# Kernel optimization log

Measured on AMD Instinct MI355X. Metric: run time of the kernel, lower is better.

The kernel has to match this reference:

```python
import jax, jax.numpy as jnp
import numpy as np

N = 50000   # nodes
E = 800000  # edges
D = 256     # in = hidden = out channels
R = 16      # num_relations (last index reserved for self-loops)
B = 8       # num_bases
LN_EPS = 1e-5


def setup_inputs() -> dict:
    key = jax.random.key(0)
    ks = jax.random.split(key, 20)
    s_basis = np.sqrt(2.0 / (D + D)).astype(np.float32)  # glorot-ish scale
    s_att = np.sqrt(2.0 / (R + B)).astype(np.float32)
    inp = {
        "x": jax.random.normal(ks[0], (N, D), dtype=jnp.float32),
        "edge_index": jax.random.randint(ks[1], (2, E), 0, N),
        "edge_type": jax.random.randint(ks[2], (E,), 0, R),
        "edge_attr": jax.random.uniform(ks[3], (E,), dtype=jnp.float32),
        # layer 1 params
        "basis1": jax.random.normal(ks[4], (B, D, D), dtype=jnp.float32) * s_basis,
        "att1": jax.random.normal(ks[5], (R, B), dtype=jnp.float32) * s_att,
        "root1": jax.random.normal(ks[6], (D, D), dtype=jnp.float32) * s_basis,
        "bias1": jnp.zeros((D,), dtype=jnp.float32),
        "ln1_g": jnp.ones((D,), dtype=jnp.float32),
        "ln1_b": jnp.zeros((D,), dtype=jnp.float32),
        # layer 2 params
        "basis2": jax.random.normal(ks[7], (B, D, D), dtype=jnp.float32) * s_basis,
        "att2": jax.random.normal(ks[8], (R, B), dtype=jnp.float32) * s_att,
        "root2": jax.random.normal(ks[9], (D, D), dtype=jnp.float32) * s_basis,
        "bias2": jnp.zeros((D,), dtype=jnp.float32),
        "ln2_g": jnp.ones((D,), dtype=jnp.float32),
        "ln2_b": jnp.zeros((D,), dtype=jnp.float32),
    }
    return inp


def _layer_norm(x, g, b):
    mu = jnp.mean(x, axis=-1, keepdims=True)
    var = jnp.mean(jnp.square(x - mu), axis=-1, keepdims=True)
    return (x - mu) * jax.lax.rsqrt(var + LN_EPS) * g + b


def _rgcn_layer(x, edge_index, edge_type, edge_attr, basis, att, root, bias):
    n = x.shape[0]
    r = att.shape[0]
    # W_r = sum_b a_rb V_b ; then per-relation transform of every node.
    weight = jnp.einsum('rb,bio->rio', att, basis)          # [R, D, D]
    H = jnp.einsum('ni,rio->nro', x, weight)                # [N, R, D]
    # append self-loops with relation index R-1 and confidence 1.0
    loop = jnp.arange(n, dtype=edge_index.dtype)
    src = jnp.concatenate([edge_index[0], loop])
    dst = jnp.concatenate([edge_index[1], loop])
    et = jnp.concatenate([edge_type, jnp.full((n,), r - 1, dtype=edge_type.dtype)])
    ea = jnp.concatenate([edge_attr, jnp.ones((n,), dtype=x.dtype)])
    msg = H[src, et] * ea[:, None]                          # [E+N, D]
    summ = jax.ops.segment_sum(msg, dst, num_segments=n)
    cnt = jax.ops.segment_sum(jnp.ones_like(ea), dst, num_segments=n)
    agg = summ / cnt[:, None]                               # scatter-mean (cnt >= 1 via self-loops)
    return agg + x @ root + bias


def reference(x, edge_index, edge_type, edge_attr,
              basis1, att1, root1, bias1, ln1_g, ln1_b,
              basis2, att2, root2, bias2, ln2_g, ln2_b):
    # input_proj / output_proj are Identity since in == hidden == out.
    h = x
    h_out = _rgcn_layer(h, edge_index, edge_type, edge_attr, basis1, att1, root1, bias1)
    h = jax.nn.relu(_layer_norm(h + h_out, ln1_g, ln1_b))
    h_out = _rgcn_layer(h, edge_index, edge_type, edge_attr, basis2, att2, root2, bias2)
    h = jax.nn.relu(_layer_norm(h + h_out, ln2_g, ln2_b))
    return h
```

## Files before the change

kernel.cpp:

```cpp
#include <hip/hip_runtime.h>
#include <stdint.h>

#define D 256
#define RREL 16
#define BB 8
#define K9 2304
#define KG 2048
#define LN_EPS 1e-5f
#define NT (K9 / 64)
#define BUFB 49152

typedef __attribute__((ext_vector_type(8))) short frag8;
typedef __attribute__((ext_vector_type(4))) float floatx4;
typedef __attribute__((ext_vector_type(2))) float float2v;

__device__ __forceinline__ unsigned short f2bf(float f) {
    union { float f; uint32_t u; } v; v.f = f;
    uint32_t r = (v.u + 0x7FFFu + ((v.u >> 16) & 1u)) >> 16;
    return (unsigned short)r;
}
__device__ __forceinline__ float bf2f(unsigned short u) {
    union { uint32_t u; float f; } v; v.u = (uint32_t)u << 16;
    return v.f;
}
__device__ __forceinline__ float2v bfpair(uint32_t d) {
    union { uint32_t u; float f; } lo, hi;
    lo.u = d << 16; hi.u = d & 0xFFFF0000u;
    return (float2v){lo.f, hi.f};
}

__device__ __forceinline__ float2v pk_mul(float2v a, float2v b) {
    float2v d;
    asm("v_pk_mul_f32 %0, %1, %2" : "=v"(d) : "v"(a), "v"(b));
    return d;
}
__device__ __forceinline__ void pk_fma_lo(float2v& acc, float2v c, float2v x) {
    asm("v_pk_fma_f32 %0, %1, %2, %0 op_sel:[0,0,0] op_sel_hi:[1,0,1]"
        : "+v"(acc) : "v"(c), "v"(x));
}
__device__ __forceinline__ void pk_fma_hi(float2v& acc, float2v c, float2v x) {
    asm("v_pk_fma_f32 %0, %1, %2, %0 op_sel:[0,1,0] op_sel_hi:[1,1,1]"
        : "+v"(acc) : "v"(c), "v"(x));
}

__device__ __forceinline__ void gl2lds16(const unsigned short* g, char* l) {
    __builtin_amdgcn_global_load_lds((const __attribute__((address_space(1))) void*)g,
                                     (__attribute__((address_space(3))) void*)l, 16, 0, 0);
}

__global__ __launch_bounds__(256) void k_cvt(const float* __restrict__ src,
                                             unsigned short* __restrict__ dst, int n4) {
    int i = blockIdx.x * 256 + threadIdx.x;
    if (i >= n4) return;
    float4 v = ((const float4*)src)[i];
    ushort4 o = make_ushort4(f2bf(v.x), f2bf(v.y), f2bf(v.z), f2bf(v.w));
    ((ushort4*)dst)[i] = o;
}

__global__ __launch_bounds__(256) void k_deg(const int* __restrict__ ei,
                                             int* __restrict__ deg, int E) {
    int t = blockIdx.x * 256 + threadIdx.x;
    int stride = gridDim.x * 256;
    int d[8];
#pragma unroll
    for (int j = 0; j < 8; ++j) {
        int e = t + j * stride;
        d[j] = (e < E) ? ei[E + e] : -1;
    }
#pragma unroll
    for (int j = 0; j < 8; ++j)
        if (d[j] >= 0) atomicAdd(&deg[d[j]], 1);
}

__global__ __launch_bounds__(256) void k_scan1(const int* __restrict__ deg,
                                               int* __restrict__ csum, int N) {
    __shared__ int sh[256];
    int n = blockIdx.x * 256 + threadIdx.x;
    sh[threadIdx.x] = (n < N) ? deg[n] : 0;
    __syncthreads();
    for (int off = 128; off > 0; off >>= 1) {
        if (threadIdx.x < off) sh[threadIdx.x] += sh[threadIdx.x + off];
        __syncthreads();
    }
    if (threadIdx.x == 0) csum[blockIdx.x] = sh[0];
}

__global__ __launch_bounds__(256) void k_scan3(const int* __restrict__ deg,
                                               const int* __restrict__ csum, int nch,
                                               int* __restrict__ rowptr,
                                               int* __restrict__ cursor,
                                               float* __restrict__ cnt, int N) {
    __shared__ int sh[256];
    int tid = threadIdx.x;
    int bid = blockIdx.x;
    int base;
    if (nch <= 256) {
        int c = (tid < nch) ? csum[tid] : 0;
        sh[tid] = c;
        __syncthreads();
        for (int off = 1; off < 256; off <<= 1) {
            int t = (tid >= off) ? sh[tid - off] : 0;
            __syncthreads();
            sh[tid] += t;
            __syncthreads();
        }
        base = sh[bid] - csum[bid];
        if (bid == 0 && tid == 255) rowptr[N] = sh[255];
        __syncthreads();
    } else {
        int s = 0;
        for (int i = 0; i < bid; ++i) s += csum[i];
        base = s;
        if (bid == 0 && tid == 0) {
            int tot = 0;
            for (int i = 0; i < nch; ++i) tot += csum[i];
            rowptr[N] = tot;
        }
    }
    int n = bid * 256 + tid;
    int v = (n < N) ? deg[n] : 0;
    sh[tid] = v;
    __syncthreads();
    for (int off = 1; off < 256; off <<= 1) {
        int t = (tid >= off) ? sh[tid - off] : 0;
        __syncthreads();
        sh[tid] += t;
        __syncthreads();
    }
    int excl = sh[tid] - v + base;
    if (n < N) {
        rowptr[n] = excl;
        cursor[n] = excl;
        cnt[n] = (float)(v + 1);
    }
}

__global__ __launch_bounds__(256) void k_scatter(const int* __restrict__ ei,
                                                 const int* __restrict__ et,
                                                 const float* __restrict__ ea,
                                                 int* __restrict__ cursor,
                                                 int2* __restrict__ ep, int E) {
    int t = blockIdx.x * 256 + threadIdx.x;
    int stride = gridDim.x * 256;
    int src[8], dst[8], typ[8]; float w[8]; bool v[8];
#pragma unroll
    for (int j = 0; j < 8; ++j) {
        int e = t + j * stride;
        v[j] = (e < E);
        if (v[j]) { src[j] = ei[e]; dst[j] = ei[E + e]; typ[j] = et[e]; w[j] = ea[e]; }
    }
    int p[8];
#pragma unroll
    for (int j = 0; j < 8; ++j)
        if (v[j]) p[j] = atomicAdd(&cursor[dst[j]], 1);
#pragma unroll
    for (int j = 0; j < 8; ++j)
        if (v[j]) ep[p[j]] = make_int2(src[j] | (typ[j] << 24), __float_as_int(w[j]));
}

__global__ __launch_bounds__(256) void k_prep_w(const float* __restrict__ basis,
                                                const float* __restrict__ root,
                                                unsigned short* __restrict__ Wt) {
    __shared__ float tile[64][65];
    int k0 = blockIdx.x * 64, o0 = blockIdx.y * 64;
    const float* src = (k0 < BB * D) ? (basis + (size_t)k0 * D)
                                     : (root + (size_t)(k0 - BB * D) * D);
    int tid = threadIdx.x;
#pragma unroll
    for (int t = 0; t < 16; ++t) {
        int idx = t * 256 + tid;
        int kk = idx >> 6, oo = idx & 63;
        tile[kk][oo] = src[(size_t)kk * D + o0 + oo];
    }
    __syncthreads();
#pragma unroll
    for (int t = 0; t < 16; ++t) {
        int idx = t * 256 + tid;
        int oo = idx >> 6, kk = idx & 63;
        Wt[(size_t)(o0 + oo) * K9 + k0 + kk] = f2bf(tile[kk][oo]);
    }
}

__device__ __forceinline__ void edge_fma(float2v g2[4][4], float2v c0, float2v c1,
                                         float2v c2, float2v c3,
                                         float2v x0, float2v x1) {
    pk_fma_lo(g2[0][0], c0, x0); pk_fma_lo(g2[1][0], c1, x0);
    pk_fma_lo(g2[2][0], c2, x0); pk_fma_lo(g2[3][0], c3, x0);
    pk_fma_hi(g2[0][1], c0, x0); pk_fma_hi(g2[1][1], c1, x0);
    pk_fma_hi(g2[2][1], c2, x0); pk_fma_hi(g2[3][1], c3, x0);
    pk_fma_lo(g2[0][2], c0, x1); pk_fma_lo(g2[1][2], c1, x1);
    pk_fma_lo(g2[2][2], c2, x1); pk_fma_lo(g2[3][2], c3, x1);
    pk_fma_hi(g2[0][3], c0, x1); pk_fma_hi(g2[1][3], c1, x1);
    pk_fma_hi(g2[2][3], c2, x1); pk_fma_hi(g2[3][3], c3, x1);
}

__device__ __forceinline__ void do_edge(float2v g2[4][4], const float* att_s,
                                        int2 pe, uint2 ud) {
    int r = (unsigned)pe.x >> 24;
    const float4* Ar = (const float4*)&att_s[r * BB];
    float4 a0 = Ar[0], a1 = Ar[1];
    float we = __int_as_float(pe.y);
    float2v w2 = {we, we};
    float2v c0 = pk_mul(w2, (float2v){a0.x, a0.y});
    float2v c1 = pk_mul(w2, (float2v){a0.z, a0.w});
    float2v c2 = pk_mul(w2, (float2v){a1.x, a1.y});
    float2v c3 = pk_mul(w2, (float2v){a1.z, a1.w});
    float2v x0 = bfpair(ud.x), x1 = bfpair(ud.y);
    edge_fma(g2, c0, c1, c2, c3, x0, x1);
}

__global__ __launch_bounds__(256) void k_gather(
    const unsigned short* __restrict__ xb, const float* __restrict__ att,
    const int* __restrict__ rowptr, const int2* __restrict__ ep,
    unsigned short* __restrict__ G, int n0, int rows, int N) {
    __shared__ __align__(32) float att_s[RREL * BB];
    int tid = threadIdx.x;
    if (tid < RREL * BB) att_s[tid] = att[tid];
    __syncthreads();
    int wv = tid >> 6, lane = tid & 63;
    int rloc = blockIdx.x * 4 + wv;
    if (rloc >= rows) return;
    int n = n0 + rloc;
    unsigned short* gout = G + (size_t)rloc * KG + lane * 4;
    if (n >= N) {
        ushort4 z = make_ushort4(0, 0, 0, 0);
#pragma unroll
        for (int b = 0; b < BB; ++b) *(ushort4*)(gout + b * D) = z;
        return;
    }
    uint2 xu = *(const uint2*)&xb[(size_t)n * D + lane * 4];
    float2v xs0 = bfpair(xu.x), xs1 = bfpair(xu.y);
    float xv[4] = {xs0.x, xs0.y, xs1.x, xs1.y};

    float2v g2[4][4];
#pragma unroll
    for (int bp = 0; bp < 4; ++bp) {
        float2v ap = {att_s[(RREL - 1) * BB + 2 * bp],
                      att_s[(RREL - 1) * BB + 2 * bp + 1]};
#pragma unroll
        for (int j = 0; j < 4; ++j) {
            float2v xs = {xv[j], xv[j]};
            g2[bp][j] = ap * xs;
        }
    }

    int e0 = rowptr[n], e1 = rowptr[n + 1];
    int e = e0;
    for (; e + 4 <= e1; e += 4) {
        int2 pa = ep[e], pb = ep[e + 1], pc = ep[e + 2], pd = ep[e + 3];
        uint2 uA = *(const uint2*)&xb[(size_t)(pa.x & 0xFFFFFF) * D + lane * 4];
        uint2 uB = *(const uint2*)&xb[(size_t)(pb.x & 0xFFFFFF) * D + lane * 4];
        uint2 uC = *(const uint2*)&xb[(size_t)(pc.x & 0xFFFFFF) * D + lane * 4];
        uint2 uD = *(const uint2*)&xb[(size_t)(pd.x & 0xFFFFFF) * D + lane * 4];
        __builtin_amdgcn_sched_barrier(0);
        do_edge(g2, att_s, pa, uA);
        do_edge(g2, att_s, pb, uB);
        do_edge(g2, att_s, pc, uC);
        do_edge(g2, att_s, pd, uD);
    }
    if (e + 2 <= e1) {
        int2 pa = ep[e], pb = ep[e + 1];
        uint2 uA = *(const uint2*)&xb[(size_t)(pa.x & 0xFFFFFF) * D + lane * 4];
        uint2 uB = *(const uint2*)&xb[(size_t)(pb.x & 0xFFFFFF) * D + lane * 4];
        __builtin_amdgcn_sched_barrier(0);
        do_edge(g2, att_s, pa, uA);
        do_edge(g2, att_s, pb, uB);
        e += 2;
    }
    if (e < e1) {
        int2 pa = ep[e];
        uint2 uA = *(const uint2*)&xb[(size_t)(pa.x & 0xFFFFFF) * D + lane * 4];
        do_edge(g2, att_s, pa, uA);
    }
#pragma unroll
    for (int bp = 0; bp < 4; ++bp) {
        ushort4 o0 = make_ushort4(f2bf(g2[bp][0].x), f2bf(g2[bp][1].x),
                                  f2bf(g2[bp][2].x), f2bf(g2[bp][3].x));
        *(ushort4*)(gout + (2 * bp) * D) = o0;
        ushort4 o1 = make_ushort4(f2bf(g2[bp][0].y), f2bf(g2[bp][1].y),
                                  f2bf(g2[bp][2].y), f2bf(g2[bp][3].y));
        *(ushort4*)(gout + (2 * bp + 1) * D) = o1;
    }
}

__global__ __launch_bounds__(1024, 4) void k_gemm(
    const unsigned short* __restrict__ G, const unsigned short* __restrict__ xb,
    const unsigned short* __restrict__ Wt,
    const float* __restrict__ hin, const float* __restrict__ cnt,
    const float* __restrict__ bias, const float* __restrict__ gln,
    const float* __restrict__ bln, float* __restrict__ hout,
    unsigned short* __restrict__ houtb, int n0, int N) {
    __shared__ __align__(16) char smem[2 * BUFB];
    float* ps   = (float*)smem;
    float* pq   = ps + 512;
    float* mu_s = ps + 1024;
    float* rs_s = ps + 1152;

    int tid = threadIdx.x;
    int wv = tid >> 6, lane = tid & 63;
    int quad = lane >> 4, l16 = lane & 15;
    int wm = wv >> 2, wn = wv & 3;
    int grow = blockIdx.x * 128;
    int nb = n0 + grow;

    int arow_s = tid >> 3, aslot_s = tid & 7;
    int swzA = (aslot_s ^ (arow_s & 7)) << 3;
    const unsigned short* gAG = G + (size_t)(grow + arow_s) * KG + swzA;
    const unsigned short* gAX = xb + (size_t)(nb + arow_s) * D + swzA;
    char* lA = smem + (tid << 4);
    const unsigned short* gB[2]; char* lB[2];
#pragma unroll
    for (int t = 0; t < 2; ++t) {
        int c = t * 1024 + tid;
        int brow = c >> 3, bslot = c & 7;
        gB[t] = Wt + (size_t)brow * K9 + ((bslot ^ (brow & 7)) << 3);
        lB[t] = smem + 16384 + (c << 4);
    }

    floatx4 acc[2][4];
    floatx4 acc2[2][4];
#pragma unroll
    for (int mf = 0; mf < 2; ++mf)
#pragma unroll
        for (int nf = 0; nf < 4; ++nf) {
            acc[mf][nf]  = (floatx4){0.f, 0.f, 0.f, 0.f};
            acc2[mf][nf] = (floatx4){0.f, 0.f, 0.f, 0.f};
        }

    auto STAGE = [&](int it, int soff) {
        const unsigned short* sa =
            (it < 32) ? (gAG + it * 64) : (gAX + (it - 32) * 64);
        gl2lds16(sa, lA + soff);
        int koff = it * 64;
        gl2lds16(gB[0] + koff, lB[0] + soff);
        gl2lds16(gB[1] + koff, lB[1] + soff);
    };
    auto COMPUTE = [&](int soff, floatx4 (&ac)[2][4]) {
        const char* Ab = smem + soff;
        const char* Bb = Ab + 16384;
#pragma unroll
        for (int kc = 0; kc < 2; ++kc) {
            int g = kc * 4 + quad;
            frag8 a[2], b[4];
#pragma unroll
            for (int mf = 0; mf < 2; ++mf) {
                int arow = wm * 32 + mf * 16 + l16;
                a[mf] = *(const frag8*)(Ab + arow * 128 + ((g ^ (arow & 7)) << 4));
            }
#pragma unroll
            for (int nf = 0; nf < 4; ++nf) {
                int brow = wn * 64 + nf * 16 + l16;
                b[nf] = *(const frag8*)(Bb + brow * 128 + ((g ^ (brow & 7)) << 4));
            }
#pragma unroll
            for (int mf = 0; mf < 2; ++mf)
#pragma unroll
                for (int nf = 0; nf < 4; ++nf)
                    ac[mf][nf] = __builtin_amdgcn_mfma_f32_16x16x32_bf16(
                        a[mf], b[nf], ac[mf][nf], 0, 0, 0);
        }
    };

    STAGE(0, 0);
    __syncthreads();
    for (int it = 0; it < 32; it += 2) {
        STAGE(it + 1, BUFB);
        COMPUTE(0, acc);
        __syncthreads();
        STAGE(it + 2, 0);
        COMPUTE(BUFB, acc);
        __syncthreads();
    }
    for (int it = 32; it < NT; it += 2) {
        STAGE(it + 1, BUFB);
        COMPUTE(0, acc2);
        __syncthreads();
        if (it + 2 < NT) STAGE(it + 2, 0);
        COMPUTE(BUFB, acc2);
        __syncthreads();
    }

    int col[4]; float bic[4];
#pragma unroll
    for (int nf = 0; nf < 4; ++nf) {
        col[nf] = wn * 64 + nf * 16 + l16;
        bic[nf] = bias[col[nf]];
    }
#pragma unroll
    for (int mf = 0; mf < 2; ++mf) {
#pragma unroll
        for (int r = 0; r < 4; ++r) {
            int row = wm * 32 + mf * 16 + quad * 4 + r;
            int n = nb + row;
            float s = 0.f, sq = 0.f;
            if (n < N) {
                float inv = 1.0f / cnt[n];
                const float* hp = hin + (size_t)n * D;
#pragma unroll
                for (int nf = 0; nf < 4; ++nf) {
                    float v = acc[mf][nf][r] * inv + acc2[mf][nf][r]
                            + hp[col[nf]] + bic[nf];
                    acc[mf][nf][r] = v;
                    s += v; sq += v * v;
                }
            }
            s += __shfl_xor(s, 1); sq += __shfl_xor(sq, 1);
            s += __shfl_xor(s, 2); sq += __shfl_xor(sq, 2);
            s += __shfl_xor(s, 4); sq += __shfl_xor(sq, 4);
            s += __shfl_xor(s, 8); sq += __shfl_xor(sq, 8);
            if (l16 == 0) {
                ps[row * 4 + wn] = s;
                pq[row * 4 + wn] = sq;
            }
        }
    }
    __syncthreads();
    if (tid < 128) {
        float s  = ps[tid * 4] + ps[tid * 4 + 1] + ps[tid * 4 + 2] + ps[tid * 4 + 3];
        float sq = pq[tid * 4] + pq[tid * 4 + 1] + pq[tid * 4 + 2] + pq[tid * 4 + 3];
        float mu = s * (1.f / D);
        mu_s[tid] = mu;
        rs_s[tid] = rsqrtf(sq * (1.f / D) - mu * mu + LN_EPS);
    }
    __syncthreads();

    float gc[4], bc[4];
#pragma unroll
    for (int nf = 0; nf < 4; ++nf) {
        gc[nf] = gln[col[nf]];
        bc[nf] = bln[col[nf]];
    }
#pragma unroll
    for (int mf = 0; mf < 2; ++mf) {
#pragma unroll
        for (int r = 0; r < 4; ++r) {
            int row = wm * 32 + mf * 16 + quad * 4 + r;
            int n = nb + row;
            if (n >= N) continue;
            float mu = mu_s[row], rs = rs_s[row];
            float* op = hout + (size_t)n * D;
#pragma unroll
            for (int nf = 0; nf < 4; ++nf) {
                float o = fmaxf((acc[mf][nf][r] - mu) * rs * gc[nf] + bc[nf], 0.f);
                op[col[nf]] = o;
                if (houtb) houtb[(size_t)n * D + col[nf]] = f2bf(o);
            }
        }
    }
}

extern "C" void kernel_launch(void* const* d_in, const int* in_sizes, int n_in,
                              void* d_out, int out_size, void* d_ws, size_t ws_size,
                              hipStream_t stream) {
    const float* x      = (const float*)d_in[0];
    const int*   ei     = (const int*)d_in[1];
    const int*   et     = (const int*)d_in[2];
    const float* ea     = (const float*)d_in[3];
    const float* basis1 = (const float*)d_in[4];
    const float* att1   = (const float*)d_in[5];
    const float* root1  = (const float*)d_in[6];
    const float* bias1  = (const float*)d_in[7];
    const float* g1     = (const float*)d_in[8];
    const float* b1     = (const float*)d_in[9];
    const float* basis2 = (const float*)d_in[10];
    const float* att2   = (const float*)d_in[11];
    const float* root2  = (const float*)d_in[12];
    const float* bias2  = (const float*)d_in[13];
    const float* g2     = (const float*)d_in[14];
    const float* b2     = (const float*)d_in[15];
    float* out = (float*)d_out;

    int N = in_sizes[0] / D;
    int E = in_sizes[2];
    int nch = (N + 255) / 256;
    int Mp = ((N + 63) / 64) * 64;
    int T = Mp / 64;
    int Tpad = (T + 1) & ~1;

    char* p = (char*)d_ws;
    size_t used = 0;
    auto alloc = [&](size_t bytes) {
        char* q = p;
        size_t a = (bytes + 255) & ~(size_t)255;
        p += a; used += a;
        return q;
    };
    float*          h1     = (float*)alloc((size_t)N * D * 4);
    unsigned short* xb     = (unsigned short*)alloc((size_t)N * D * 2);
    unsigned short* h1b    = (unsigned short*)alloc((size_t)N * D * 2);
    unsigned short* Wt     = (unsigned short*)alloc((size_t)K9 * D * 2);
    int*            deg    = (int*)alloc((size_t)N * 4);
    int*            rowptr = (int*)alloc((size_t)(N + 1) * 4);
    int*            cursor = (int*)alloc((size_t)N * 4);
    float*          cnt    = (float*)alloc((size_t)N * 4);
    int2*           ep     = (int2*)alloc((size_t)E * 8);
    int*            csum   = (int*)alloc((size_t)nch * 4);
    size_t remain = (ws_size > used + 256) ? (ws_size - used - 256) : 0;
    size_t tile_bytes = (size_t)64 * KG * 2;
    int ct_max = (int)(remain / tile_bytes);
    if (ct_max < 2) ct_max = 2;
    if (ct_max > Tpad) ct_max = Tpad;
    unsigned short* G = (unsigned short*)alloc((size_t)ct_max * tile_bytes);

    int nch2 = (Tpad + ct_max - 1) / ct_max;
    int ct = (Tpad + nch2 - 1) / nch2;
    ct = (ct + 1) & ~1;
    if (ct > ct_max) ct = ct_max & ~1;
    if (ct < 2) ct = 2;

    hipMemsetAsync(deg, 0, (size_t)N * 4, stream);
    int gE8 = (E + 2047) / 2048;
    k_deg<<<gE8, 256, 0, stream>>>(ei, deg, E);
    k_scan1<<<nch, 256, 0, stream>>>(deg, csum, N);
    k_scan3<<<nch, 256, 0, stream>>>(deg, csum, nch, rowptr, cursor, cnt, N);
    k_scatter<<<gE8, 256, 0, stream>>>(ei, et, ea, cursor, ep, E);
    k_cvt<<<(N * D / 4 + 255) / 256, 256, 0, stream>>>(x, xb, N * D / 4);

    const float* bas[2]  = {basis1, basis2};
    const float* attp[2] = {att1, att2};
    const float* rt[2]   = {root1, root2};
    const float* bi[2]   = {bias1, bias2};
    const float* lg[2]   = {g1, g2};
    const float* lb[2]   = {b1, b2};
    const unsigned short* gin[2] = {xb, h1b};
    const float* hres[2] = {x, h1};
    float*          hof[2] = {h1, out};
    unsigned short* hob[2] = {h1b, nullptr};

    for (int L = 0; L < 2; ++L) {
        k_prep_w<<<dim3(K9 / 64, D / 64), 256, 0, stream>>>(bas[L], rt[L], Wt);
        for (int c0 = 0; c0 < Tpad; c0 += ct) {
            int tiles = (Tpad - c0 < ct) ? (Tpad - c0) : ct;
            int rows = tiles * 64;
            int n0 = c0 * 64;
            k_gather<<<rows / 4, 256, 0, stream>>>(gin[L], attp[L], rowptr, ep,
                                                   G, n0, rows, N);
            k_gemm<<<rows / 128, 1024, 0, stream>>>(G, gin[L], Wt, hres[L], cnt,
                                                    bi[L], lg[L], lb[L], hof[L],
                                                    hob[L], n0, N);
        }
    }
}
```

Measured before the change: 618.0 us.

## Fold mean normalization into gather, merge accumulators, drop fp32 intermediate when workspace allows

After: 618.2 us. No clear change (+0.0%).

```diff
diff --git a/kernel.cpp b/kernel.cpp
--- a/kernel.cpp
+++ b/kernel.cpp
@@ -212,6 +212,7 @@
 __global__ __launch_bounds__(256) void k_gather(
     const unsigned short* __restrict__ xb, const float* __restrict__ att,
     const int* __restrict__ rowptr, const int2* __restrict__ ep,
+    const float* __restrict__ cnt,
     unsigned short* __restrict__ G, int n0, int rows, int N) {
     __shared__ __align__(32) float att_s[RREL * BB];
     int tid = threadIdx.x;
@@ -272,13 +273,17 @@
         uint2 uA = *(const uint2*)&xb[(size_t)(pa.x & 0xFFFFFF) * D + lane * 4];
         do_edge(g2, att_s, pa, uA);
     }
+    float inv = 1.0f / cnt[n];
+    float2v inv2 = {inv, inv};
 #pragma unroll
     for (int bp = 0; bp < 4; ++bp) {
-        ushort4 o0 = make_ushort4(f2bf(g2[bp][0].x), f2bf(g2[bp][1].x),
-                                  f2bf(g2[bp][2].x), f2bf(g2[bp][3].x));
+        float2v v0 = pk_mul(inv2, g2[bp][0]);
+        float2v v1 = pk_mul(inv2, g2[bp][1]);
+        float2v v2 = pk_mul(inv2, g2[bp][2]);
+        float2v v3 = pk_mul(inv2, g2[bp][3]);
+        ushort4 o0 = make_ushort4(f2bf(v0.x), f2bf(v1.x), f2bf(v2.x), f2bf(v3.x));
         *(ushort4*)(gout + (2 * bp) * D) = o0;
-        ushort4 o1 = make_ushort4(f2bf(g2[bp][0].y), f2bf(g2[bp][1].y),
-                                  f2bf(g2[bp][2].y), f2bf(g2[bp][3].y));
+        ushort4 o1 = make_ushort4(f2bf(v0.y), f2bf(v1.y), f2bf(v2.y), f2bf(v3.y));
         *(ushort4*)(gout + (2 * bp + 1) * D) = o1;
     }
 }
@@ -286,7 +291,7 @@
 __global__ __launch_bounds__(1024, 4) void k_gemm(
     const unsigned short* __restrict__ G, const unsigned short* __restrict__ xb,
     const unsigned short* __restrict__ Wt,
-    const float* __restrict__ hin, const float* __restrict__ cnt,
+    const float* __restrict__ hinf, const unsigned short* __restrict__ hinb,
     const float* __restrict__ bias, const float* __restrict__ gln,
     const float* __restrict__ bln, float* __restrict__ hout,
     unsigned short* __restrict__ houtb, int n0, int N) {
@@ -318,14 +323,11 @@
     }
 
     floatx4 acc[2][4];
-    floatx4 acc2[2][4];
 #pragma unroll
     for (int mf = 0; mf < 2; ++mf)
 #pragma unroll
-        for (int nf = 0; nf < 4; ++nf) {
-            acc[mf][nf]  = (floatx4){0.f, 0.f, 0.f, 0.f};
-            acc2[mf][nf] = (floatx4){0.f, 0.f, 0.f, 0.f};
-        }
+        for (int nf = 0; nf < 4; ++nf)
+            acc[mf][nf] = (floatx4){0.f, 0.f, 0.f, 0.f};
 
     auto STAGE = [&](int it, int soff) {
         const unsigned short* sa =
@@ -335,7 +337,7 @@
         gl2lds16(gB[0] + koff, lB[0] + soff);
         gl2lds16(gB[1] + koff, lB[1] + soff);
     };
-    auto COMPUTE = [&](int soff, floatx4 (&ac)[2][4]) {
+    auto COMPUTE = [&](int soff) {
         const char* Ab = smem + soff;
         const char* Bb = Ab + 16384;
 #pragma unroll
@@ -356,27 +358,19 @@
             for (int mf = 0; mf < 2; ++mf)
 #pragma unroll
                 for (int nf = 0; nf < 4; ++nf)
-                    ac[mf][nf] = __builtin_amdgcn_mfma_f32_16x16x32_bf16(
-                        a[mf], b[nf], ac[mf][nf], 0, 0, 0);
+                    acc[mf][nf] = __builtin_amdgcn_mfma_f32_16x16x32_bf16(
+                        a[mf], b[nf], acc[mf][nf], 0, 0, 0);
         }
     };
 
     STAGE(0, 0);
     __syncthreads();
-    for (int it = 0; it < 32; it += 2) {
+    for (int it = 0; it < NT; it += 2) {
         STAGE(it + 1, BUFB);
-        COMPUTE(0, acc);
-        __syncthreads();
-        STAGE(it + 2, 0);
-        COMPUTE(BUFB, acc);
-        __syncthreads();
-    }
-    for (int it = 32; it < NT; it += 2) {
-        STAGE(it + 1, BUFB);
-        COMPUTE(0, acc2);
+        COMPUTE(0);
         __syncthreads();
         if (it + 2 < NT) STAGE(it + 2, 0);
-        COMPUTE(BUFB, acc2);
+        COMPUTE(BUFB);
         __syncthreads();
     }
 
@@ -394,12 +388,12 @@
             int n = nb + row;
             float s = 0.f, sq = 0.f;
             if (n < N) {
-                float inv = 1.0f / cnt[n];
-                const float* hp = hin + (size_t)n * D;
+                const float* hpf = hinf ? hinf + (size_t)n * D : nullptr;
+                const unsigned short* hpb = hinb ? hinb + (size_t)n * D : nullptr;
 #pragma unroll
                 for (int nf = 0; nf < 4; ++nf) {
-                    float v = acc[mf][nf][r] * inv + acc2[mf][nf][r]
-                            + hp[col[nf]] + bic[nf];
+                    float res = hpf ? hpf[col[nf]] : bf2f(hpb[col[nf]]);
+                    float v = acc[mf][nf][r] + res + bic[nf];
                     acc[mf][nf][r] = v;
                     s += v; sq += v * v;
                 }
@@ -438,11 +432,10 @@
             int n = nb + row;
             if (n >= N) continue;
             float mu = mu_s[row], rs = rs_s[row];
-            float* op = hout + (size_t)n * D;
 #pragma unroll
             for (int nf = 0; nf < 4; ++nf) {
                 float o = fmaxf((acc[mf][nf][r] - mu) * rs * gc[nf] + bc[nf], 0.f);
-                op[col[nf]] = o;
+                if (hout)  hout[(size_t)n * D + col[nf]] = o;
                 if (houtb) houtb[(size_t)n * D + col[nf]] = f2bf(o);
             }
         }
@@ -485,7 +478,6 @@
         p += a; used += a;
         return q;
     };
-    float*          h1     = (float*)alloc((size_t)N * D * 4);
     unsigned short* xb     = (unsigned short*)alloc((size_t)N * D * 2);
     unsigned short* h1b    = (unsigned short*)alloc((size_t)N * D * 2);
     unsigned short* Wt     = (unsigned short*)alloc((size_t)K9 * D * 2);
@@ -495,18 +487,27 @@
     float*          cnt    = (float*)alloc((size_t)N * 4);
     int2*           ep     = (int2*)alloc((size_t)E * 8);
     int*            csum   = (int*)alloc((size_t)nch * 4);
+
+    size_t tile_bytes = (size_t)64 * KG * 2;
     size_t remain = (ws_size > used + 256) ? (ws_size - used - 256) : 0;
-    size_t tile_bytes = (size_t)64 * KG * 2;
-    int ct_max = (int)(remain / tile_bytes);
-    if (ct_max < 2) ct_max = 2;
-    if (ct_max > Tpad) ct_max = Tpad;
-    unsigned short* G = (unsigned short*)alloc((size_t)ct_max * tile_bytes);
-
-    int nch2 = (Tpad + ct_max - 1) / ct_max;
-    int ct = (Tpad + nch2 - 1) / nch2;
-    ct = (ct + 1) & ~1;
-    if (ct > ct_max) ct = ct_max & ~1;
-    if (ct < 2) ct = 2;
+
+    float* h1 = nullptr;
+    int ct;
+    if (remain >= (size_t)Tpad * tile_bytes) {
+        ct = Tpad;
+    } else {
+        h1 = (float*)alloc((size_t)N * D * 4);
+        remain = (ws_size > used + 256) ? (ws_size - used - 256) : 0;
+        int ct_max = (int)(remain / tile_bytes);
+        if (ct_max < 2) ct_max = 2;
+        if (ct_max > Tpad) ct_max = Tpad;
+        int nch2 = (Tpad + ct_max - 1) / ct_max;
+        ct = (Tpad + nch2 - 1) / nch2;
+        ct = (ct + 1) & ~1;
+        if (ct > ct_max) ct = ct_max & ~1;
+        if (ct < 2) ct = 2;
+    }
+    unsigned short* G = (unsigned short*)alloc((size_t)ct * tile_bytes);
 
     hipMemsetAsync(deg, 0, (size_t)N * 4, stream);
     int gE8 = (E + 2047) / 2048;
@@ -523,7 +524,8 @@
     const float* lg[2]   = {g1, g2};
     const float* lb[2]   = {b1, b2};
     const unsigned short* gin[2] = {xb, h1b};
-    const float* hres[2] = {x, h1};
+    const float*          hrf[2] = {x, h1};
+    const unsigned short* hrb[2] = {nullptr, h1 ? nullptr : h1b};
     float*          hof[2] = {h1, out};
     unsigned short* hob[2] = {h1b, nullptr};
 
@@ -534,8 +536,8 @@
             int rows = tiles * 64;
             int n0 = c0 * 64;
             k_gather<<<rows / 4, 256, 0, stream>>>(gin[L], attp[L], rowptr, ep,
-                                                   G, n0, rows, N);
-            k_gemm<<<rows / 128, 1024, 0, stream>>>(G, gin[L], Wt, hres[L], cnt,
+                                                   cnt, G, n0, rows, N);
+            k_gemm<<<rows / 128, 1024, 0, stream>>>(G, gin[L], Wt, hrf[L], hrb[L],
                                                     bi[L], lg[L], lb[L], hof[L],
                                                     hob[L], n0, N);
         }
```
